# Kernel tuning notes

Measured on AMD Instinct MI355X. Metric: run time of the kernel, lower is better.

Reference implementation:

```python
import jax, jax.numpy as jnp
import numpy as np

WS = 7          # window size (height == width)
NUM_HEADS = 16


def _rel_pos_index(ws: int) -> np.ndarray:
    # Mirrors get_relative_position_index with q_windows == k_windows == (ws, ws).
    coords = np.stack(np.meshgrid(np.arange(ws), np.arange(ws), indexing='ij'))  # (2, ws, ws)
    flat = coords.reshape(2, -1)                                                 # (2, N)
    rel = flat[:, :, None] - flat[:, None, :]                                    # (2, N, N)
    rel = rel.transpose(1, 2, 0).astype(np.int64)                                # (N, N, 2)
    rel[:, :, 0] += ws - 1
    rel[:, :, 1] += ws - 1
    rel[:, :, 0] *= 2 * ws - 1
    return rel.sum(-1)  # (N, N), values in [0, (2*ws-1)^2)


def setup_inputs() -> dict:
    key = jax.random.key(0)
    ks = jax.random.split(key, 6)
    nWB, N, C = 1024, WS * WS, 512
    x = jax.random.normal(ks[0], (nWB, N, C), dtype=jnp.float32)
    qkv_w = jax.random.normal(ks[1], (C, 3 * C), dtype=jnp.float32) * 0.02
    qkv_b = jnp.zeros((3 * C,), dtype=jnp.float32)
    rel_pos_bias_table = jax.random.normal(ks[2], ((2 * WS - 1) ** 2, NUM_HEADS), dtype=jnp.float32) * 0.02
    proj_w = jax.random.normal(ks[3], (C, C), dtype=jnp.float32) * 0.02
    proj_b = jnp.zeros((C,), dtype=jnp.float32)
    return {"x": x, "qkv_w": qkv_w, "qkv_b": qkv_b,
            "rel_pos_bias_table": rel_pos_bias_table,
            "proj_w": proj_w, "proj_b": proj_b}


def reference(x, qkv_w, qkv_b, rel_pos_bias_table, proj_w, proj_b):
    # x: (nW*B, N, C) window tokens
    nWB, N, C = x.shape
    h = NUM_HEADS
    d = C // h
    scale = d ** -0.5

    qkv = x @ qkv_w + qkv_b                          # (nWB, N, 3C)
    qkv = qkv.reshape(nWB, N, 3, h, d).transpose(2, 0, 3, 1, 4)  # (3, nWB, h, N, d)
    q, k, v = qkv[0], qkv[1], qkv[2]

    attn = jnp.einsum('bhqd,bhkd->bhqk', q * scale, k)           # (nWB, h, N, N)

    rel_idx = jnp.asarray(_rel_pos_index(WS))                    # (N, N) constant
    bias = rel_pos_bias_table[rel_idx]                           # (N, N, h)
    attn = attn + bias.transpose(2, 0, 1)[None]                  # broadcast over windows

    attn = jax.nn.softmax(attn, axis=-1)
    out = jnp.einsum('bhqk,bhkd->bhqd', attn, v)                 # (nWB, h, N, d)
    out = out.transpose(0, 2, 1, 3).reshape(nWB, N, C)
    out = out @ proj_w + proj_b
    return out
```

## Files before the change

kernel.cpp:

```cpp
#include <hip/hip_runtime.h>
#include <hip/hip_bf16.h>

typedef __attribute__((ext_vector_type(4))) float f32x4;
typedef __attribute__((ext_vector_type(8))) short s16x8;

#define MFMA16(a,b,c) __builtin_amdgcn_mfma_f32_16x16x32_bf16(a,b,c,0,0,0)

__device__ __forceinline__ unsigned short f2bf(float f){
  __hip_bfloat16 h = __float2bfloat16(f);
  return *reinterpret_cast<unsigned short*>(&h);
}

__device__ __forceinline__ s16x8 cvt8(f32x4 a, f32x4 b){
  s16x8 t;
  t[0]=(short)f2bf(a[0]); t[1]=(short)f2bf(a[1]);
  t[2]=(short)f2bf(a[2]); t[3]=(short)f2bf(a[3]);
  t[4]=(short)f2bf(b[0]); t[5]=(short)f2bf(b[1]);
  t[6]=(short)f2bf(b[2]); t[7]=(short)f2bf(b[3]);
  return t;
}

__device__ __forceinline__ void gload_lds16(const unsigned short* g, unsigned short* l){
  __builtin_amdgcn_global_load_lds(
      (const __attribute__((address_space(1))) unsigned int*)(const void*)g,
      (__attribute__((address_space(3))) unsigned int*)(void*)l,
      16, 0, 0);
}

__global__ void k_prep2(const float* __restrict__ x,
                        const float* __restrict__ qkv_w,
                        const float* __restrict__ qkv_b,
                        const float* __restrict__ proj_w,
                        const float* __restrict__ btab,
                        unsigned short* __restrict__ xb,
                        unsigned short* __restrict__ wqkv_t,
                        unsigned short* __restrict__ wproj_t,
                        float* __restrict__ bqkv_s,
                        float* __restrict__ bias_t)
{
  if (blockIdx.x < 12544){
    const int i = blockIdx.x * 256 + threadIdx.x;
    const float* p = x + (size_t)i*8;
    f32x4 v0 = *(const f32x4*)p, v1 = *(const f32x4*)(p+4);
    *(s16x8*)(xb + (size_t)i*8) = cvt8(v0, v1);
    return;
  }
  const float scale = 0.17677669529663687f;
  int tid = (blockIdx.x - 12544) * 256 + threadIdx.x;
  int np  = 512 * 256;
  for (int i = tid; i < 1536*512; i += np){
    int c = i >> 9, k = i & 511;
    float w = qkv_w[k*1536 + c];
    if (c < 512) w *= scale;
    wqkv_t[i] = f2bf(w);
  }
  for (int i = tid; i < 512*512; i += np){
    int c = i >> 9, k = i & 511;
    wproj_t[i] = f2bf(proj_w[k*512 + c]);
  }
  for (int i = tid; i < 1536; i += np){
    float bv = qkv_b[i];
    if (i < 512) bv *= scale;
    bqkv_s[i] = bv;
  }
  for (int i = tid; i < 16*64*64; i += np){
    int hh = i >> 12, rc = i & 4095, row = rc >> 6, col = rc & 63;
    float v;
    if (col >= 49)      v = -1e30f;
    else if (row >= 49) v = 0.f;
    else {
      int qy = row/7, qx = row%7, ky = col/7, kx = col%7;
      v = btab[((qy-ky+6)*13 + (qx-kx+6))*16 + hh];
    }
    bias_t[i] = v;
  }
}

__global__ __launch_bounds__(256) void k_qkv2(
    const unsigned short* __restrict__ xb,
    const unsigned short* __restrict__ wqkv_t,
    const float* __restrict__ bqkv_s,
    unsigned short* __restrict__ qkvb)
{
  __shared__ unsigned short lds[16384];
  const int t    = threadIdx.x;
  const int lane = t & 63;
  const int wave = t >> 6;
  const int l16  = lane & 15;
  const int lg   = lane >> 4;
  const int wr   = wave >> 1;
  const int wc   = wave & 1;
  const f32x4 ZERO4 = {0.f, 0.f, 0.f, 0.f};

  const int bid  = blockIdx.x;
  const int xcd  = bid & 7;
  const int idx  = bid >> 3;
  const int nb   = idx % 12;
  const int mgrp = idx / 12;
  const int mb   = xcd*49 + mgrp;
  const int m0   = mb * 128;
  const int n0   = nb * 128;

  const int srow = t >> 2;
  const int scol = (t & 3) * 8;
  const unsigned short* asrc = xb     + (size_t)(m0 + srow)*512 + scol;
  const unsigned short* bsrc = wqkv_t + (size_t)(n0 + srow)*512 + scol;

  gload_lds16(asrc,          lds + wave*512);
  gload_lds16(asrc + 32768,  lds + 2048 + wave*512);
  gload_lds16(bsrc,          lds + 8192 + wave*512);
  gload_lds16(bsrc + 32768,  lds + 8192 + 2048 + wave*512);
  __syncthreads();

  f32x4 acc[4][4];
  #pragma unroll
  for (int rt=0;rt<4;++rt)
    #pragma unroll
    for (int ct=0;ct<4;++ct)
      acc[rt][ct] = ZERO4;

  #pragma unroll 2
  for (int ks = 0; ks < 16; ++ks){
    const int p = ks & 1;
    unsigned short* Ab = lds + p*4096;
    unsigned short* Bb = lds + 8192 + p*4096;

    if (ks < 15){
      const int q = (ks+1) & 1;
      const unsigned short* a2 = asrc + (ks+1)*32;
      const unsigned short* b2 = bsrc + (ks+1)*32;
      gload_lds16(a2,         lds + q*4096 + wave*512);
      gload_lds16(a2 + 32768, lds + q*4096 + 2048 + wave*512);
      gload_lds16(b2,         lds + 8192 + q*4096 + wave*512);
      gload_lds16(b2 + 32768, lds + 8192 + q*4096 + 2048 + wave*512);
    }

    s16x8 af[4], bf[4];
    #pragma unroll
    for (int rt=0;rt<4;++rt)
      af[rt] = *(const s16x8*)&Ab[(wr*64 + rt*16 + l16)*32 + lg*8];
    #pragma unroll
    for (int ct=0;ct<4;++ct)
      bf[ct] = *(const s16x8*)&Bb[(wc*64 + ct*16 + l16)*32 + lg*8];

    #pragma unroll
    for (int rt=0;rt<4;++rt)
      #pragma unroll
      for (int ct=0;ct<4;++ct)
        acc[rt][ct] = MFMA16(af[rt], bf[ct], acc[rt][ct]);

    __syncthreads();
  }

  #pragma unroll
  for (int ct=0;ct<4;++ct){
    const int col = n0 + wc*64 + ct*16 + l16;
    const float bv = bqkv_s[col];
    #pragma unroll
    for (int rt=0;rt<4;++rt){
      const int row = m0 + wr*64 + rt*16 + lg*4;
      #pragma unroll
      for (int r=0;r<4;++r)
        qkvb[(size_t)(row+r)*1536 + col] = f2bf(acc[rt][ct][r] + bv);
    }
  }
}

__global__ __launch_bounds__(256, 3) void k_attn2(
    const unsigned short* __restrict__ qkvb,
    const float* __restrict__ bias_t,
    unsigned short* __restrict__ att)
{
  __shared__ unsigned short lds[4*6656];
  const int lane = threadIdx.x & 63;
  const int wave = threadIdx.x >> 6;
  const int bid  = blockIdx.x;
  const int xcd  = bid & 7;
  const int g    = (bid >> 3) & 3;
  const int wblk = bid >> 5;
  const int b    = xcd + (wblk << 3);
  const int h    = (g << 2) | wave;
  const int l16  = lane & 15;
  const int lg   = lane >> 4;
  const f32x4 ZERO4 = {0.f, 0.f, 0.f, 0.f};

  unsigned short* p_lds = lds + wave*6656;
  unsigned short* vT    = p_lds + 4608;
  const size_t wbase = (size_t)b * 49;

  for (int i = lane; i < 15*32; i += 64) vT[49*32 + i] = 0;

  s16x8 aq[4], bk[4];
  #pragma unroll
  for (int rt=0;rt<4;++rt){
    const int n = rt*16 + l16;
    s16x8 z = {0,0,0,0,0,0,0,0};
    aq[rt] = z; bk[rt] = z;
    if (n < 49){
      const unsigned short* qp = qkvb + (wbase + n)*1536 + h*32 + lg*8;
      aq[rt] = *(const s16x8*)qp;
      bk[rt] = *(const s16x8*)(qp + 512);
    }
  }

  {
    const int tokb = lane >> 2;
    const int sc   = (lane & 3) * 8;
    #pragma unroll
    for (int i=0;i<4;++i){
      const int tok = i*16 + tokb;
      if (tok < 49)
        gload_lds16(qkvb + (wbase + tok)*1536 + 1024 + h*32 + sc,
                    vT + i*512);
    }
  }

  f32x4 sacc[4][4];
  #pragma unroll
  for (int rt=0;rt<4;++rt)
    #pragma unroll
    for (int ct=0;ct<4;++ct)
      sacc[rt][ct] = MFMA16(aq[rt], bk[ct], ZERO4);

  const float* biash = bias_t + (h << 12);
  float pm[4][4];
  #pragma unroll
  for (int rt=0;rt<4;++rt){
    #pragma unroll
    for (int r=0;r<4;++r){
      const int row = rt*16 + lg*4 + r;
      const float* brow = biash + (row << 6) + l16;
      float s0 = sacc[rt][0][r] + brow[0];
      float s1 = sacc[rt][1][r] + brow[16];
      float s2 = sacc[rt][2][r] + brow[32];
      float s3 = sacc[rt][3][r] + brow[48];
      sacc[rt][0][r]=s0; sacc[rt][1][r]=s1; sacc[rt][2][r]=s2; sacc[rt][3][r]=s3;
      pm[rt][r] = fmaxf(fmaxf(s0,s1), fmaxf(s2,s3));
    }
  }
  #pragma unroll
  for (int d=1; d<16; d<<=1)
    #pragma unroll
    for (int rt=0;rt<4;++rt)
      #pragma unroll
      for (int r=0;r<4;++r)
        pm[rt][r] = fmaxf(pm[rt][r], __shfl_xor(pm[rt][r], d));

  float ps[4][4];
  #pragma unroll
  for (int rt=0;rt<4;++rt){
    #pragma unroll
    for (int r=0;r<4;++r){
      const float m = pm[rt][r];
      float e0 = __expf(sacc[rt][0][r]-m), e1 = __expf(sacc[rt][1][r]-m);
      float e2 = __expf(sacc[rt][2][r]-m), e3 = __expf(sacc[rt][3][r]-m);
      sacc[rt][0][r]=e0; sacc[rt][1][r]=e1; sacc[rt][2][r]=e2; sacc[rt][3][r]=e3;
      ps[rt][r] = e0+e1+e2+e3;
    }
  }
  #pragma unroll
  for (int d=1; d<16; d<<=1)
    #pragma unroll
    for (int rt=0;rt<4;++rt)
      #pragma unroll
      for (int r=0;r<4;++r)
        ps[rt][r] += __shfl_xor(ps[rt][r], d);

  #pragma unroll
  for (int rt=0;rt<4;++rt){
    #pragma unroll
    for (int r=0;r<4;++r){
      const int row = rt*16 + lg*4 + r;
      const float inv = 1.f / ps[rt][r];
      p_lds[row*72 +      l16] = f2bf(sacc[rt][0][r]*inv);
      p_lds[row*72 + 16 + l16] = f2bf(sacc[rt][1][r]*inv);
      p_lds[row*72 + 32 + l16] = f2bf(sacc[rt][2][r]*inv);
      p_lds[row*72 + 48 + l16] = f2bf(sacc[rt][3][r]*inv);
    }
  }

  asm volatile("s_waitcnt vmcnt(0) lgkmcnt(0)" ::: "memory");
  __builtin_amdgcn_sched_barrier(0);

  f32x4 oacc[4][2];
  #pragma unroll
  for (int rt=0;rt<4;++rt)
    #pragma unroll
    for (int ct=0;ct<2;++ct)
      oacc[rt][ct] = ZERO4;

  #pragma unroll
  for (int kt=0; kt<2; ++kt){
    s16x8 ap[4], bv2[2];
    #pragma unroll
    for (int rt=0;rt<4;++rt)
      ap[rt] = *(const s16x8*)&p_lds[(rt*16+l16)*72 + kt*32 + lg*8];
    #pragma unroll
    for (int ct=0;ct<2;++ct){
      s16x8 fr;
      #pragma unroll
      for (int j=0;j<8;++j)
        fr[j] = (short)vT[(kt*32 + lg*8 + j)*32 + ct*16 + l16];
      bv2[ct] = fr;
    }
    #pragma unroll
    for (int rt=0;rt<4;++rt)
      #pragma unroll
      for (int ct=0;ct<2;++ct)
        oacc[rt][ct] = MFMA16(ap[rt], bv2[ct], oacc[rt][ct]);
  }

  unsigned short* o_lds = p_lds;
  #pragma unroll
  for (int rt=0;rt<4;++rt)
    #pragma unroll
    for (int ct=0;ct<2;++ct){
      const int row0 = rt*16 + lg*4;
      f32x4 vv = oacc[rt][ct];
      #pragma unroll
      for (int r=0;r<4;++r)
        o_lds[(row0+r)*40 + ct*16 + l16] = f2bf(vv[r]);
    }
  unsigned short* attb = att + (size_t)b*49*512 + h*32;
  for (int i = lane; i < 49*4; i += 64){
    const int row = i >> 2, seg = i & 3;
    *(s16x8*)&attb[(size_t)row*512 + seg*8] = *(const s16x8*)&o_lds[row*40 + seg*8];
  }
}

__global__ __launch_bounds__(256) void k_proj2(
    const unsigned short* __restrict__ att,
    const unsigned short* __restrict__ wproj_t,
    const float* __restrict__ proj_b,
    float* __restrict__ out)
{
  __shared__ unsigned short lds[16384];
  const int t    = threadIdx.x;
  const int lane = t & 63;
  const int wave = t >> 6;
  const int l16  = lane & 15;
  const int lg   = lane >> 4;
  const int wr   = wave >> 1;
  const int wc   = wave & 1;
  const f32x4 ZERO4 = {0.f, 0.f, 0.f, 0.f};

  const int bid  = blockIdx.x;
  const int xcd  = bid & 7;
  const int idx  = bid >> 3;
  const int nb   = idx & 3;
  const int mgrp = idx >> 2;
  const int mb   = xcd*49 + mgrp;
  const int m0   = mb * 128;
  const int n0   = nb * 128;

  const int srow = t >> 2;
  const int scol = (t & 3) * 8;
  const unsigned short* asrc = att     + (size_t)(m0 + srow)*512 + scol;
  const unsigned short* bsrc = wproj_t + (size_t)(n0 + srow)*512 + scol;

  gload_lds16(asrc,          lds + wave*512);
  gload_lds16(asrc + 32768,  lds + 2048 + wave*512);
  gload_lds16(bsrc,          lds + 8192 + wave*512);
  gload_lds16(bsrc + 32768,  lds + 8192 + 2048 + wave*512);
  __syncthreads();

  f32x4 acc[4][4];
  #pragma unroll
  for (int rt=0;rt<4;++rt)
    #pragma unroll
    for (int ct=0;ct<4;++ct)
      acc[rt][ct] = ZERO4;

  #pragma unroll 2
  for (int ks = 0; ks < 16; ++ks){
    const int p = ks & 1;
    unsigned short* Ab = lds + p*4096;
    unsigned short* Bb = lds + 8192 + p*4096;

    if (ks < 15){
      const int q = (ks+1) & 1;
      const unsigned short* a2 = asrc + (ks+1)*32;
      const unsigned short* b2 = bsrc + (ks+1)*32;
      gload_lds16(a2,         lds + q*4096 + wave*512);
      gload_lds16(a2 + 32768, lds + q*4096 + 2048 + wave*512);
      gload_lds16(b2,         lds + 8192 + q*4096 + wave*512);
      gload_lds16(b2 + 32768, lds + 8192 + q*4096 + 2048 + wave*512);
    }

    s16x8 af[4], bf[4];
    #pragma unroll
    for (int rt=0;rt<4;++rt)
      af[rt] = *(const s16x8*)&Ab[(wr*64 + rt*16 + l16)*32 + lg*8];
    #pragma unroll
    for (int ct=0;ct<4;++ct)
      bf[ct] = *(const s16x8*)&Bb[(wc*64 + ct*16 + l16)*32 + lg*8];

    #pragma unroll
    for (int rt=0;rt<4;++rt)
      #pragma unroll
      for (int ct=0;ct<4;++ct)
        acc[rt][ct] = MFMA16(af[rt], bf[ct], acc[rt][ct]);

    __syncthreads();
  }

  #pragma unroll
  for (int ct=0;ct<4;++ct){
    const int col = n0 + wc*64 + ct*16 + l16;
    const float bv = proj_b[col];
    #pragma unroll
    for (int rt=0;rt<4;++rt){
      const int row = m0 + wr*64 + rt*16 + lg*4;
      #pragma unroll
      for (int r=0;r<4;++r)
        out[(size_t)(row+r)*512 + col] = acc[rt][ct][r] + bv;
    }
  }
}

__global__ __launch_bounds__(256, 3) void k_qkv_attn8(
    const unsigned short* __restrict__ xb,
    const unsigned short* __restrict__ wqkv_t,
    const float* __restrict__ bqkv_s,
    const float* __restrict__ bias_t,
    unsigned short* __restrict__ att)
{
  __shared__ unsigned short lds[4*5120 + 2*2048];
  const int lane = threadIdx.x & 63;
  const int wave = threadIdx.x >> 6;
  const int bid  = blockIdx.x;
  const int xcd  = bid & 7;
  const int g    = (bid >> 3) & 3;
  const int wblk = bid >> 5;
  const int b    = xcd + (wblk << 3);
  const int h    = (g << 2) | wave;
  const int l16  = lane & 15;
  const int lg   = lane >> 4;
  const f32x4 ZERO4 = {0.f, 0.f, 0.f, 0.f};

  unsigned short* q_lds  = lds + wave*5120;
  unsigned short* k_lds  = q_lds + 2560;
  unsigned short* p_lds  = q_lds;
  unsigned short* xstage = lds + 4*5120;

  for (int i = threadIdx.x; i < 2*15*32; i += 256){
    int bf = i / 480, rem = i % 480;
    xstage[bf*2048 + (49 + rem/32)*32 + (rem & 31)] = 0;
  }

  const unsigned short* xwin = xb + (size_t)b*49*512;
  const int srow = wave*16 + (lane>>2);
  const int cbase = h * 32;
  const unsigned short* xsrc = xwin + (size_t)srow*512 + (lane&3)*8;
  const unsigned short* bbase = wqkv_t + (size_t)(cbase + l16)*512 + lg*8;

  __syncthreads();
  if (srow < 49) gload_lds16(xsrc, xstage + wave*512);
  __syncthreads();

  f32x4 acc[3][4][2];
  #pragma unroll
  for (int a=0;a<3;++a)
    #pragma unroll
    for (int rt=0;rt<4;++rt)
      #pragma unroll
      for (int ct=0;ct<2;++ct)
        acc[a][rt][ct] = ZERO4;

  #pragma unroll 2
  for (int ks = 0; ks < 16; ++ks){
    const int p = ks & 1;
    s16x8 bfrag[6];
    #pragma unroll
    for (int wq=0; wq<3; ++wq)
      #pragma unroll
      for (int ct=0; ct<2; ++ct)
        bfrag[wq*2+ct] = *(const s16x8*)(bbase + wq*262144 + ct*8192 + ks*32);

    if (ks < 15 && srow < 49)
      gload_lds16(xsrc + (ks+1)*32, xstage + ((ks+1)&1)*2048 + wave*512);

    s16x8 afrag[4];
    #pragma unroll
    for (int rt=0; rt<4; ++rt)
      afrag[rt] = *(const s16x8*)&xstage[p*2048 + (rt*16 + l16)*32 + lg*8];

    #pragma unroll
    for (int wq=0;wq<3;++wq)
      #pragma unroll
      for (int rt=0;rt<4;++rt)
        #pragma unroll
        for (int ct=0;ct<2;++ct)
          acc[wq][rt][ct] = MFMA16(afrag[rt], bfrag[wq*2+ct], acc[wq][rt][ct]);

    __syncthreads();
  }

  uint2 vpk[4][2];
  #pragma unroll
  for (int wq=0; wq<3; ++wq){
    #pragma unroll
    for (int ct=0; ct<2; ++ct){
      const int c = wq*512 + cbase + ct*16 + l16;
      const float bv = bqkv_s[c];
      #pragma unroll
      for (int rt=0; rt<4; ++rt){
        f32x4 vv = acc[wq][rt][ct];
        const int row0 = rt*16 + lg*4;
        if (wq == 0){
          #pragma unroll
          for (int r=0;r<4;++r) q_lds[(row0+r)*40 + ct*16 + l16] = f2bf(vv[r]+bv);
        } else if (wq == 1){
          #pragma unroll
          for (int r=0;r<4;++r) k_lds[(row0+r)*40 + ct*16 + l16] = f2bf(vv[r]+bv);
        } else {
          uint2 pk;
          pk.x = (unsigned)f2bf(vv[0]+bv) | ((unsigned)f2bf(vv[1]+bv) << 16);
          pk.y = (unsigned)f2bf(vv[2]+bv) | ((unsigned)f2bf(vv[3]+bv) << 16);
          vpk[rt][ct] = pk;
        }
      }
    }
  }

  s16x8 aq[4], bk[4];
  #pragma unroll
  for (int t=0;t<4;++t){
    aq[t] = *(const s16x8*)&q_lds[(t*16+l16)*40 + lg*8];
    bk[t] = *(const s16x8*)&k_lds[(t*16+l16)*40 + lg*8];
  }
  f32x4 sacc[4][4];
  #pragma unroll
  for (int rt=0;rt<4;++rt)
    #pragma unroll
    for (int ct=0;ct<4;++ct)
      sacc[rt][ct] = MFMA16(aq[rt], bk[ct], ZERO4);

  const float* biash = bias_t + (h << 12);
  float pm[4][4];
  #pragma unroll
  for (int rt=0;rt<4;++rt){
    #pragma unroll
    for (int r=0;r<4;++r){
      const int row = rt*16 + lg*4 + r;
      const float* brow = biash + (row << 6) + l16;
      float s0 = sacc[rt][0][r] + brow[0];
      float s1 = sacc[rt][1][r] + brow[16];
      float s2 = sacc[rt][2][r] + brow[32];
      float s3 = sacc[rt][3][r] + brow[48];
      sacc[rt][0][r]=s0; sacc[rt][1][r]=s1; sacc[rt][2][r]=s2; sacc[rt][3][r]=s3;
      pm[rt][r] = fmaxf(fmaxf(s0,s1), fmaxf(s2,s3));
    }
  }
  #pragma unroll
  for (int d=1; d<16; d<<=1)
    #pragma unroll
    for (int rt=0;rt<4;++rt)
      #pragma unroll
      for (int r=0;r<4;++r)
        pm[rt][r] = fmaxf(pm[rt][r], __shfl_xor(pm[rt][r], d));

  float ps[4][4];
  #pragma unroll
  for (int rt=0;rt<4;++rt){
    #pragma unroll
    for (int r=0;r<4;++r){
      const float m = pm[rt][r];
      float e0 = __expf(sacc[rt][0][r]-m), e1 = __expf(sacc[rt][1][r]-m);
      float e2 = __expf(sacc[rt][2][r]-m), e3 = __expf(sacc[rt][3][r]-m);
      sacc[rt][0][r]=e0; sacc[rt][1][r]=e1; sacc[rt][2][r]=e2; sacc[rt][3][r]=e3;
      ps[rt][r] = e0+e1+e2+e3;
    }
  }
  #pragma unroll
  for (int d=1; d<16; d<<=1)
    #pragma unroll
    for (int rt=0;rt<4;++rt)
      #pragma unroll
      for (int r=0;r<4;++r)
        ps[rt][r] += __shfl_xor(ps[rt][r], d);

  #pragma unroll
  for (int rt=0;rt<4;++rt){
    #pragma unroll
    for (int r=0;r<4;++r){
      const int row = rt*16 + lg*4 + r;
      const float inv = 1.f / ps[rt][r];
      p_lds[row*72 +      l16] = f2bf(sacc[rt][0][r]*inv);
      p_lds[row*72 + 16 + l16] = f2bf(sacc[rt][1][r]*inv);
      p_lds[row*72 + 32 + l16] = f2bf(sacc[rt][2][r]*inv);
      p_lds[row*72 + 48 + l16] = f2bf(sacc[rt][3][r]*inv);
    }
  }

  const int srcA = l16 + ((lg & 1) << 5);
  const int srcB = srcA + 16;
  const bool hiSel = (lg >> 1) != 0;

  f32x4 oacc[4][2];
  #pragma unroll
  for (int rt=0;rt<4;++rt)
    #pragma unroll
    for (int ct=0;ct<2;++ct)
      oacc[rt][ct] = ZERO4;

  #pragma unroll
  for (int kt=0; kt<2; ++kt){
    s16x8 ap[4], bv2[2];
    #pragma unroll
    for (int rt=0;rt<4;++rt)
      ap[rt] = *(const s16x8*)&p_lds[(rt*16+l16)*72 + kt*32 + lg*8];
    #pragma unroll
    for (int ct=0;ct<2;++ct){
      unsigned a0x = (unsigned)__shfl((int)vpk[2*kt  ][ct].x, srcA, 64);
      unsigned a0y = (unsigned)__shfl((int)vpk[2*kt  ][ct].y, srcA, 64);
      unsigned a1x = (unsigned)__shfl((int)vpk[2*kt+1][ct].x, srcA, 64);
      unsigned a1y = (unsigned)__shfl((int)vpk[2*kt+1][ct].y, srcA, 64);
      unsigned b0x = (unsigned)__shfl((int)vpk[2*kt  ][ct].x, srcB, 64);
      unsigned b0y = (unsigned)__shfl((int)vpk[2*kt  ][ct].y, srcB, 64);
      unsigned b1x = (unsigned)__shfl((int)vpk[2*kt+1][ct].x, srcB, 64);
      unsigned b1y = (unsigned)__shfl((int)vpk[2*kt+1][ct].y, srcB, 64);
      union { s16x8 v; unsigned u[4]; } fr;
      fr.u[0] = hiSel ? a1x : a0x;
      fr.u[1] = hiSel ? a1y : a0y;
      fr.u[2] = hiSel ? b1x : b0x;
      fr.u[3] = hiSel ? b1y : b0y;
      bv2[ct] = fr.v;
    }
    #pragma unroll
    for (int rt=0;rt<4;++rt)
      #pragma unroll
      for (int ct=0;ct<2;++ct)
        oacc[rt][ct] = MFMA16(ap[rt], bv2[ct], oacc[rt][ct]);
  }

  unsigned short* o_lds = p_lds;
  #pragma unroll
  for (int rt=0;rt<4;++rt)
    #pragma unroll
    for (int ct=0;ct<2;++ct){
      const int row0 = rt*16 + lg*4;
      f32x4 vv = oacc[rt][ct];
      #pragma unroll
      for (int r=0;r<4;++r)
        o_lds[(row0+r)*40 + ct*16 + l16] = f2bf(vv[r]);
    }
  unsigned short* attb = att + (size_t)b*49*512 + h*32;
  for (int i = lane; i < 49*4; i += 64){
    const int row = i >> 2, seg = i & 3;
    *(s16x8*)&attb[(size_t)row*512 + seg*8] = *(const s16x8*)&o_lds[row*40 + seg*8];
  }
}

extern "C" void kernel_launch(void* const* d_in, const int* in_sizes, int n_in,
                              void* d_out, int out_size, void* d_ws, size_t ws_size,
                              hipStream_t stream)
{
  const float* x      = (const float*)d_in[0];
  const float* qkv_w  = (const float*)d_in[1];
  const float* qkv_b  = (const float*)d_in[2];
  const float* btab   = (const float*)d_in[3];
  const float* proj_w = (const float*)d_in[4];
  const float* proj_b = (const float*)d_in[5];
  float* out = (float*)d_out;

  char* ws = (char*)d_ws;
  const size_t QKV = 154140672ULL;
  const size_t ATT = 51380224ULL;
  const size_t WQ  = 1572864ULL;
  const size_t WP  = 524288ULL;
  const size_t BT  = 262144ULL;
  const size_t need_new = ATT + QKV + WQ + WP + BT + 8192;
  const size_t need_big = ATT + ATT + WQ + WP + BT + 8192;

  if (ws_size >= need_new){
    unsigned short* attxb   = (unsigned short*)ws;
    unsigned short* qkvb    = (unsigned short*)(ws + ATT);
    unsigned short* wqkv_t  = (unsigned short*)(ws + ATT + QKV);
    unsigned short* wproj_t = (unsigned short*)(ws + ATT + QKV + WQ);
    float*          bias_t  = (float*)(ws + ATT + QKV + WQ + WP);
    float*          bqkv_s  = (float*)(ws + ATT + QKV + WQ + WP + BT);

    k_prep2<<<12544 + 512, 256, 0, stream>>>(x, qkv_w, qkv_b, proj_w, btab,
                                             attxb, wqkv_t, wproj_t, bqkv_s, bias_t);
    k_qkv2<<<4704, 256, 0, stream>>>(attxb, wqkv_t, bqkv_s, qkvb);
    k_attn2<<<4096, 256, 0, stream>>>(qkvb, bias_t, attxb);
    k_proj2<<<1568, 256, 0, stream>>>(attxb, wproj_t, proj_b, out);
  } else {
    unsigned short* att     = (unsigned short*)ws;
    unsigned short* xbb     = (unsigned short*)(ws + ATT);
    unsigned short* wqkv_t  = (unsigned short*)(ws + ATT + ATT);
    unsigned short* wproj_t = (unsigned short*)(ws + ATT + ATT + WQ);
    float*          bias_t  = (float*)(ws + ATT + ATT + WQ + WP);
    float*          bqkv_s  = (float*)(ws + ATT + ATT + WQ + WP + BT);

    k_prep2<<<12544 + 512, 256, 0, stream>>>(x, qkv_w, qkv_b, proj_w, btab,
                                             xbb, wqkv_t, wproj_t, bqkv_s, bias_t);
    k_qkv_attn8<<<1024*4, 256, 0, stream>>>(xbb, wqkv_t, bqkv_s, bias_t, att);
    k_proj2<<<392*4, 256, 0, stream>>>(att, wproj_t, proj_b, out);
  }
}
```

Baseline: 245.6 us.

## Triple-buffer GEMM K-loop with vmcnt waits and single barrier per step

The QKV and projection GEMM kernels move from double-buffered LDS staging to a three-stage ring. Each step waits on vmcnt for the oldest stage, then issues one barrier instead of two syncthreads, and the K loop is fully unrolled. The attention kernel now issues its V global-to-LDS loads before the Q/K register loads so they overlap. LDS per block grows from 32KB to 48KB, which may lower occupancy, and the hand-written vmcnt counts depend on the compiler not reordering memory ops.

```diff
diff --git a/kernel.cpp b/kernel.cpp
--- a/kernel.cpp
+++ b/kernel.cpp
@@ -76,13 +76,13 @@
   }
 }
 
-__global__ __launch_bounds__(256) void k_qkv2(
+__global__ __launch_bounds__(256) void k_qkv3(
     const unsigned short* __restrict__ xb,
     const unsigned short* __restrict__ wqkv_t,
     const float* __restrict__ bqkv_s,
     unsigned short* __restrict__ qkvb)
 {
-  __shared__ unsigned short lds[16384];
+  __shared__ unsigned short lds[24576];
   const int t    = threadIdx.x;
   const int lane = t & 63;
   const int wave = t >> 6;
@@ -106,11 +106,17 @@
   const unsigned short* asrc = xb     + (size_t)(m0 + srow)*512 + scol;
   const unsigned short* bsrc = wqkv_t + (size_t)(n0 + srow)*512 + scol;
 
-  gload_lds16(asrc,          lds + wave*512);
-  gload_lds16(asrc + 32768,  lds + 2048 + wave*512);
-  gload_lds16(bsrc,          lds + 8192 + wave*512);
-  gload_lds16(bsrc + 32768,  lds + 8192 + 2048 + wave*512);
-  __syncthreads();
+#define STAGE_Q(T, BUF) {                                                  \
+    const unsigned short* a2_ = asrc + (T)*32;                             \
+    const unsigned short* b2_ = bsrc + (T)*32;                             \
+    gload_lds16(a2_,         lds + (BUF)*4096 + wave*512);                 \
+    gload_lds16(a2_ + 32768, lds + (BUF)*4096 + 2048 + wave*512);          \
+    gload_lds16(b2_,         lds + 12288 + (BUF)*4096 + wave*512);         \
+    gload_lds16(b2_ + 32768, lds + 12288 + (BUF)*4096 + 2048 + wave*512);  \
+  }
+
+  STAGE_Q(0, 0)
+  STAGE_Q(1, 1)
 
   f32x4 acc[4][4];
   #pragma unroll
@@ -119,22 +125,18 @@
     for (int ct=0;ct<4;++ct)
       acc[rt][ct] = ZERO4;
 
-  #pragma unroll 2
+  #pragma unroll
   for (int ks = 0; ks < 16; ++ks){
-    const int p = ks & 1;
+    if (ks < 15) asm volatile("s_waitcnt vmcnt(4)" ::: "memory");
+    else         asm volatile("s_waitcnt vmcnt(0)" ::: "memory");
+    __builtin_amdgcn_s_barrier();
+    __builtin_amdgcn_sched_barrier(0);
+
+    if (ks + 2 < 16) STAGE_Q(ks + 2, (ks + 2) % 3)
+
+    const int p = ks % 3;
     unsigned short* Ab = lds + p*4096;
-    unsigned short* Bb = lds + 8192 + p*4096;
-
-    if (ks < 15){
-      const int q = (ks+1) & 1;
-      const unsigned short* a2 = asrc + (ks+1)*32;
-      const unsigned short* b2 = bsrc + (ks+1)*32;
-      gload_lds16(a2,         lds + q*4096 + wave*512);
-      gload_lds16(a2 + 32768, lds + q*4096 + 2048 + wave*512);
-      gload_lds16(b2,         lds + 8192 + q*4096 + wave*512);
-      gload_lds16(b2 + 32768, lds + 8192 + q*4096 + 2048 + wave*512);
-    }
-
+    unsigned short* Bb = lds + 12288 + p*4096;
     s16x8 af[4], bf[4];
     #pragma unroll
     for (int rt=0;rt<4;++rt)
@@ -148,9 +150,8 @@
       #pragma unroll
       for (int ct=0;ct<4;++ct)
         acc[rt][ct] = MFMA16(af[rt], bf[ct], acc[rt][ct]);
-
-    __syncthreads();
-  }
+  }
+#undef STAGE_Q
 
   #pragma unroll
   for (int ct=0;ct<4;++ct){
@@ -190,6 +191,18 @@
 
   for (int i = lane; i < 15*32; i += 64) vT[49*32 + i] = 0;
 
+  {
+    const int tokb = lane >> 2;
+    const int sc   = (lane & 3) * 8;
+    #pragma unroll
+    for (int i=0;i<4;++i){
+      const int tok = i*16 + tokb;
+      if (tok < 49)
+        gload_lds16(qkvb + (wbase + tok)*1536 + 1024 + h*32 + sc,
+                    vT + i*512);
+    }
+  }
+
   s16x8 aq[4], bk[4];
   #pragma unroll
   for (int rt=0;rt<4;++rt){
@@ -200,18 +213,6 @@
       const unsigned short* qp = qkvb + (wbase + n)*1536 + h*32 + lg*8;
       aq[rt] = *(const s16x8*)qp;
       bk[rt] = *(const s16x8*)(qp + 512);
-    }
-  }
-
-  {
-    const int tokb = lane >> 2;
-    const int sc   = (lane & 3) * 8;
-    #pragma unroll
-    for (int i=0;i<4;++i){
-      const int tok = i*16 + tokb;
-      if (tok < 49)
-        gload_lds16(qkvb + (wbase + tok)*1536 + 1024 + h*32 + sc,
-                    vT + i*512);
     }
   }
 
@@ -328,13 +329,13 @@
   }
 }
 
-__global__ __launch_bounds__(256) void k_proj2(
+__global__ __launch_bounds__(256) void k_proj3(
     const unsigned short* __restrict__ att,
     const unsigned short* __restrict__ wproj_t,
     const float* __restrict__ proj_b,
     float* __restrict__ out)
 {
-  __shared__ unsigned short lds[16384];
+  __shared__ unsigned short lds[24576];
   const int t    = threadIdx.x;
   const int lane = t & 63;
   const int wave = t >> 6;
@@ -358,11 +359,17 @@
   const unsigned short* asrc = att     + (size_t)(m0 + srow)*512 + scol;
   const unsigned short* bsrc = wproj_t + (size_t)(n0 + srow)*512 + scol;
 
-  gload_lds16(asrc,          lds + wave*512);
-  gload_lds16(asrc + 32768,  lds + 2048 + wave*512);
-  gload_lds16(bsrc,          lds + 8192 + wave*512);
-  gload_lds16(bsrc + 32768,  lds + 8192 + 2048 + wave*512);
-  __syncthreads();
+#define STAGE_P(T, BUF) {                                                  \
+    const unsigned short* a2_ = asrc + (T)*32;                             \
+    const unsigned short* b2_ = bsrc + (T)*32;                             \
+    gload_lds16(a2_,         lds + (BUF)*4096 + wave*512);                 \
+    gload_lds16(a2_ + 32768, lds + (BUF)*4096 + 2048 + wave*512);          \
+    gload_lds16(b2_,         lds + 12288 + (BUF)*4096 + wave*512);         \
+    gload_lds16(b2_ + 32768, lds + 12288 + (BUF)*4096 + 2048 + wave*512);  \
+  }
+
+  STAGE_P(0, 0)
+  STAGE_P(1, 1)
 
   f32x4 acc[4][4];
   #pragma unroll
@@ -371,22 +378,18 @@
     for (int ct=0;ct<4;++ct)
       acc[rt][ct] = ZERO4;
 
-  #pragma unroll 2
+  #pragma unroll
   for (int ks = 0; ks < 16; ++ks){
-    const int p = ks & 1;
+    if (ks < 15) asm volatile("s_waitcnt vmcnt(4)" ::: "memory");
+    else         asm volatile("s_waitcnt vmcnt(0)" ::: "memory");
+    __builtin_amdgcn_s_barrier();
+    __builtin_amdgcn_sched_barrier(0);
+
+    if (ks + 2 < 16) STAGE_P(ks + 2, (ks + 2) % 3)
+
+    const int p = ks % 3;
     unsigned short* Ab = lds + p*4096;
-    unsigned short* Bb = lds + 8192 + p*4096;
-
-    if (ks < 15){
-      const int q = (ks+1) & 1;
-      const unsigned short* a2 = asrc + (ks+1)*32;
-      const unsigned short* b2 = bsrc + (ks+1)*32;
-      gload_lds16(a2,         lds + q*4096 + wave*512);
-      gload_lds16(a2 + 32768, lds + q*4096 + 2048 + wave*512);
-      gload_lds16(b2,         lds + 8192 + q*4096 + wave*512);
-      gload_lds16(b2 + 32768, lds + 8192 + q*4096 + 2048 + wave*512);
-    }
-
+    unsigned short* Bb = lds + 12288 + p*4096;
     s16x8 af[4], bf[4];
     #pragma unroll
     for (int rt=0;rt<4;++rt)
@@ -400,9 +403,8 @@
       #pragma unroll
       for (int ct=0;ct<4;++ct)
         acc[rt][ct] = MFMA16(af[rt], bf[ct], acc[rt][ct]);
-
-    __syncthreads();
-  }
+  }
+#undef STAGE_P
 
   #pragma unroll
   for (int ct=0;ct<4;++ct){
@@ -683,9 +685,9 @@
 
     k_prep2<<<12544 + 512, 256, 0, stream>>>(x, qkv_w, qkv_b, proj_w, btab,
                                              attxb, wqkv_t, wproj_t, bqkv_s, bias_t);
-    k_qkv2<<<4704, 256, 0, stream>>>(attxb, wqkv_t, bqkv_s, qkvb);
+    k_qkv3<<<4704, 256, 0, stream>>>(attxb, wqkv_t, bqkv_s, qkvb);
     k_attn2<<<4096, 256, 0, stream>>>(qkvb, bias_t, attxb);
-    k_proj2<<<1568, 256, 0, stream>>>(attxb, wproj_t, proj_b, out);
+    k_proj3<<<1568, 256, 0, stream>>>(attxb, wproj_t, proj_b, out);
   } else {
     unsigned short* att     = (unsigned short*)ws;
     unsigned short* xbb     = (unsigned short*)(ws + ATT);
@@ -697,6 +699,6 @@
     k_prep2<<<12544 + 512, 256, 0, stream>>>(x, qkv_w, qkv_b, proj_w, btab,
                                              xbb, wqkv_t, wproj_t, bqkv_s, bias_t);
     k_qkv_attn8<<<1024*4, 256, 0, stream>>>(xbb, wqkv_t, bqkv_s, bias_t, att);
-    k_proj2<<<392*4, 256, 0, stream>>>(att, wproj_t, proj_b, out);
-  }
-}
+    k_proj3<<<392*4, 256, 0, stream>>>(att, wproj_t, proj_b, out);
+  }
+}
```

Result: faster. 228.2 us (-7.1%).
